# Kernel optimization log

Measured on AMD Instinct MI355X. Metric: run time of the kernel, lower is better.

## Reference

```python
import jax, jax.numpy as jnp
import numpy as np

N_NODES = 50000
N_EDGES = 800000
NUM_FEATURES = 128
HIDDEN = 128


def _gcn_conv(x, src, dst, norm, W, b, num_nodes):
    # x: [N, F_in], W: [F_in, F_out]
    h = x @ W                              # dense transform first (PyG order)
    msg = h[src] * norm[:, None]           # gather + per-edge scale
    out = jax.ops.segment_sum(msg, dst, num_segments=num_nodes)  # scatter-add
    return out + b


def _prep_edges(edge_index, num_nodes):
    # add self loops
    loop = jnp.arange(num_nodes, dtype=edge_index.dtype)
    src = jnp.concatenate([edge_index[0], loop])
    dst = jnp.concatenate([edge_index[1], loop])
    # symmetric normalization deg^{-1/2}[src] * deg^{-1/2}[dst]
    deg = jax.ops.segment_sum(jnp.ones_like(dst, dtype=jnp.float32), dst,
                              num_segments=num_nodes)
    dinv = jnp.where(deg > 0, jax.lax.rsqrt(deg), 0.0)
    norm = dinv[src] * dinv[dst]
    return src, dst, norm


def setup_inputs() -> dict:
    key = jax.random.key(0)
    ks = jax.random.split(key, 5)
    s1 = 1.0 / np.sqrt(NUM_FEATURES)
    s2 = 1.0 / np.sqrt(HIDDEN)
    return {
        "x": jax.random.normal(ks[0], (N_NODES, NUM_FEATURES), jnp.float32),
        "edge_index": jax.random.randint(ks[1], (2, N_EDGES), 0, N_NODES,
                                         dtype=jnp.int64),
        "W1": jax.random.normal(ks[2], (NUM_FEATURES, HIDDEN), jnp.float32) * s1,
        "b1": jnp.zeros((HIDDEN,), jnp.float32),
        "W2": jax.random.normal(ks[3], (HIDDEN, HIDDEN), jnp.float32) * s2,
        "b2": jnp.zeros((HIDDEN,), jnp.float32),
        "Wout": jax.random.normal(ks[4], (HIDDEN, 1), jnp.float32) * s2,
        "bout": jnp.zeros((1,), jnp.float32),
    }


def reference(x, edge_index, W1, b1, W2, b2, Wout, bout):
    num_nodes = x.shape[0]
    src, dst, norm = _prep_edges(edge_index, num_nodes)
    h = _gcn_conv(x, src, dst, norm, W1, b1, num_nodes)
    h = jax.nn.relu(h)
    h = _gcn_conv(h, src, dst, norm, W2, b2, num_nodes)
    h = jax.nn.relu(h)
    return jax.nn.sigmoid(h @ Wout + bout)
```

## Files before the change

### kernel.cpp

```cpp
#include <hip/hip_runtime.h>
#include <math.h>

#define NN 50000
#define NE 800000
#define NBUK 196
#define PBLK 256
#define EPB (NE / PBLK)

typedef __attribute__((ext_vector_type(8))) short bf16x8;
typedef __attribute__((ext_vector_type(4))) float f32x4;

__device__ __forceinline__ unsigned short f2b(float f) {
  union { float f; unsigned u; } v; v.f = f;
  unsigned r = v.u + 0x7FFF + ((v.u >> 16) & 1);
  return (unsigned short)(r >> 16);
}
__device__ __forceinline__ float plo(unsigned v) {
  union { unsigned u; float f; } t; t.u = v << 16; return t.f;
}
__device__ __forceinline__ float phi(unsigned v) {
  union { unsigned u; float f; } t; t.u = v & 0xFFFF0000u; return t.f;
}

__device__ __forceinline__ int edge_val(const void* ei, long long idx, int is64) {
  if (is64) return (int)((const long long*)ei)[idx];
  return ((const int*)ei)[idx];
}

__global__ __launch_bounds__(256) void k_phist(const void* __restrict__ ei,
                                               int* __restrict__ bh) {
  __shared__ int hist[NBUK];
  __shared__ int sflag;
  if (threadIdx.x < 64) {
    unsigned v = ((const unsigned*)ei)[2 * threadIdx.x + 1];
    unsigned long long m = __ballot(v == 0u);
    if (threadIdx.x == 0) sflag = (m == ~0ull) ? 1 : 0;
  }
  if (threadIdx.x < NBUK) hist[threadIdx.x] = 0;
  __syncthreads();
  int is64 = sflag;
  int base = blockIdx.x * EPB;
  for (int e = base + threadIdx.x; e < base + EPB; e += 256) {
    int d = edge_val(ei, (long long)NE + e, is64);
    atomicAdd(&hist[d >> 8], 1);
  }
  __syncthreads();
  if (threadIdx.x < NBUK) bh[threadIdx.x * PBLK + blockIdx.x] = hist[threadIdx.x];
}

__global__ __launch_bounds__(256) void k_pscanA(int* __restrict__ bh,
                                                int* __restrict__ colsum) {
  __shared__ int sh[256];
  int k = blockIdx.x, t = threadIdx.x;
  int v = bh[k * PBLK + t];
  sh[t] = v;
  __syncthreads();
  for (int s = 1; s < 256; s <<= 1) {
    int u = (t >= s) ? sh[t - s] : 0;
    __syncthreads();
    sh[t] += u;
    __syncthreads();
  }
  bh[k * PBLK + t] = sh[t] - v;
  if (t == 255) colsum[k] = sh[255];
}

__global__ __launch_bounds__(256) void k_pscanB(const int* __restrict__ colsum,
                                                int* __restrict__ bstart) {
  __shared__ int sh[256];
  int t = threadIdx.x;
  sh[t] = (t < NBUK) ? colsum[t] : 0;
  __syncthreads();
  for (int s = 1; s < 256; s <<= 1) {
    int u = (t >= s) ? sh[t - s] : 0;
    __syncthreads();
    sh[t] += u;
    __syncthreads();
  }
  if (t <= NBUK) bstart[t] = (t == 0) ? 0 : sh[t - 1];
}

__global__ __launch_bounds__(256) void k_pscat(const void* __restrict__ ei,
                                               const int* __restrict__ bh,
                                               const int* __restrict__ bstart,
                                               unsigned* __restrict__ epk) {
  __shared__ int cur[NBUK];
  __shared__ int sflag;
  if (threadIdx.x < 64) {
    unsigned v = ((const unsigned*)ei)[2 * threadIdx.x + 1];
    unsigned long long m = __ballot(v == 0u);
    if (threadIdx.x == 0) sflag = (m == ~0ull) ? 1 : 0;
  }
  if (threadIdx.x < NBUK)
    cur[threadIdx.x] = bstart[threadIdx.x] + bh[threadIdx.x * PBLK + blockIdx.x];
  __syncthreads();
  int is64 = sflag;
  int base = blockIdx.x * EPB;
  for (int e = base + threadIdx.x; e < base + EPB; e += 256) {
    int d = edge_val(ei, (long long)NE + e, is64);
    int s = edge_val(ei, e, is64);
    int p = atomicAdd(&cur[d >> 8], 1);
    epk[p] = (unsigned)s | ((unsigned)(d & 255) << 16);
  }
}

__global__ __launch_bounds__(256) void k_bofffill(const unsigned* __restrict__ epk,
                                                  const int* __restrict__ bstart,
                                                  int* __restrict__ off,
                                                  float* __restrict__ dinv,
                                                  unsigned short* __restrict__ csr16) {
  __shared__ int hist[256];
  __shared__ int cur[256];
  int k = blockIdx.x, t = threadIdx.x;
  hist[t] = 0;
  __syncthreads();
  int e0 = bstart[k], e1 = bstart[k + 1];
  for (int e = e0 + t; e < e1; e += 256)
    atomicAdd(&hist[(epk[e] >> 16) & 255], 1);
  __syncthreads();
  int myc = hist[t];
  for (int s = 1; s < 256; s <<= 1) {
    int u = (t >= s) ? hist[t - s] : 0;
    __syncthreads();
    hist[t] += u;
    __syncthreads();
  }
  int excl = hist[t] - myc;
  int node = k * 256 + t;
  if (node < NN) {
    off[node] = e0 + excl;
    dinv[node] = rsqrtf((float)(myc + 1));
  }
  cur[t] = e0 + excl;
  __syncthreads();
  for (int e = e0 + t; e < e1; e += 256) {
    unsigned pk = epk[e];
    int p = atomicAdd(&cur[(pk >> 16) & 255], 1);
    csr16[p] = (unsigned short)(pk & 0xFFFFu);
  }
  if (k == 0 && t == 0) off[NN] = NE;
}

__global__ __launch_bounds__(256) void k_wt2(const float* __restrict__ W1,
                                             const float* __restrict__ W2,
                                             unsigned short* __restrict__ Wt1,
                                             unsigned short* __restrict__ Wt2) {
  int i = blockIdx.x * 256 + threadIdx.x;
  int sel = i >> 14;
  int j = i & 16383;
  int k = j >> 7, n = j & 127;
  const float* W = sel ? W2 : W1;
  unsigned short* Wt = sel ? Wt2 : Wt1;
  Wt[n * 128 + k] = f2b(W[j]);
}

template <int A_F32>
__global__ __launch_bounds__(256, 2) void k_mgemm(const void* __restrict__ Ap,
                                                  const unsigned short* __restrict__ Wt,
                                                  const float* __restrict__ dinv,
                                                  unsigned short* __restrict__ Out,
                                                  int M) {
  int wid  = (blockIdx.x * blockDim.x + threadIdx.x) >> 6;
  int lane = threadIdx.x & 63;
  int nw   = (gridDim.x * blockDim.x) >> 6;
  int r  = lane & 15;
  int kg = lane >> 4;
  bf16x8 wf[8][4];
#pragma unroll
  for (int n = 0; n < 8; ++n)
#pragma unroll
    for (int kk = 0; kk < 4; ++kk)
      wf[n][kk] = *(const bf16x8*)&Wt[(n * 16 + r) * 128 + kk * 32 + kg * 8];
  int nstr = M >> 4;
  for (int s = wid; s < nstr; s += nw) {
    int row = s * 16 + r;
    bf16x8 xf[4];
    if (A_F32) {
      const float* Ar = (const float*)Ap + (long long)row * 128 + kg * 8;
#pragma unroll
      for (int kk = 0; kk < 4; ++kk) {
        float4 lo4 = *(const float4*)(Ar + kk * 32);
        float4 hi4 = *(const float4*)(Ar + kk * 32 + 4);
        bf16x8 t;
        t[0] = (short)f2b(lo4.x); t[1] = (short)f2b(lo4.y);
        t[2] = (short)f2b(lo4.z); t[3] = (short)f2b(lo4.w);
        t[4] = (short)f2b(hi4.x); t[5] = (short)f2b(hi4.y);
        t[6] = (short)f2b(hi4.z); t[7] = (short)f2b(hi4.w);
        xf[kk] = t;
      }
    } else {
      const unsigned short* Ar = (const unsigned short*)Ap + (long long)row * 128 + kg * 8;
#pragma unroll
      for (int kk = 0; kk < 4; ++kk)
        xf[kk] = *(const bf16x8*)(Ar + kk * 32);
    }
    f32x4 acc[8];
#pragma unroll
    for (int n = 0; n < 8; ++n) acc[n] = (f32x4){0.f, 0.f, 0.f, 0.f};
#pragma unroll
    for (int kk = 0; kk < 4; ++kk)
#pragma unroll
      for (int n = 0; n < 8; ++n)
        acc[n] = __builtin_amdgcn_mfma_f32_16x16x32_bf16(wf[n][kk], xf[kk], acc[n], 0, 0, 0);
    float dv = dinv[row];
    unsigned short* Or = Out + (long long)row * 128 + kg * 4;
#pragma unroll
    for (int n = 0; n < 8; ++n) {
      uint2 o;
      o.x = (unsigned)f2b(acc[n][0] * dv) | ((unsigned)f2b(acc[n][1] * dv) << 16);
      o.y = (unsigned)f2b(acc[n][2] * dv) | ((unsigned)f2b(acc[n][3] * dv) << 16);
      *(uint2*)(Or + n * 16) = o;
    }
  }
}

template <int FINAL>
__global__ __launch_bounds__(256) void k_agg(const unsigned short* __restrict__ Tb,
                                             const int* __restrict__ off,
                                             const unsigned short* __restrict__ csr16,
                                             const float* __restrict__ dinv,
                                             const float* __restrict__ bias,
                                             const float* __restrict__ wout,
                                             const float* __restrict__ bout,
                                             void* __restrict__ outp) {
  const uint2* Tw2 = (const uint2*)Tb;
  int wid  = (blockIdx.x * blockDim.x + threadIdx.x) >> 6;
  int lane = threadIdx.x & 63;
  int half = lane >> 5;
  int li   = lane & 31;
  int nw   = (gridDim.x * blockDim.x) >> 6;
  float4 b4 = ((const float4*)bias)[li];
  float4 w4 = make_float4(0.f, 0.f, 0.f, 0.f);
  if (FINAL) w4 = ((const float4*)wout)[li];
  for (int d = wid; d < NN; d += nw) {
    int e0 = off[d], e1 = off[d + 1];
    int np  = (e1 - e0) >> 1;
    int rem = (e1 - e0) & 1;
    int s_init = half ? (rem ? (int)csr16[e1 - 1] : -1) : d;
    float a0 = 0.f, a1 = 0.f, a2 = 0.f, a3 = 0.f;
    if (s_init >= 0) {
      uint2 vv = Tw2[s_init * 32 + li];
      a0 = plo(vv.x); a1 = phi(vv.x); a2 = plo(vv.y); a3 = phi(vv.y);
    }
    int st = 0;
    int base = e0 + half;
    for (; st + 4 <= np; st += 4) {
      int s0 = csr16[base + 2 * st];
      int s1 = csr16[base + 2 * st + 2];
      int s2 = csr16[base + 2 * st + 4];
      int s3 = csr16[base + 2 * st + 6];
      uint2 v0 = Tw2[s0 * 32 + li];
      uint2 v1 = Tw2[s1 * 32 + li];
      uint2 v2 = Tw2[s2 * 32 + li];
      uint2 v3 = Tw2[s3 * 32 + li];
      a0 += plo(v0.x); a1 += phi(v0.x); a2 += plo(v0.y); a3 += phi(v0.y);
      a0 += plo(v1.x); a1 += phi(v1.x); a2 += plo(v1.y); a3 += phi(v1.y);
      a0 += plo(v2.x); a1 += phi(v2.x); a2 += plo(v2.y); a3 += phi(v2.y);
      a0 += plo(v3.x); a1 += phi(v3.x); a2 += plo(v3.y); a3 += phi(v3.y);
    }
    for (; st < np; ++st) {
      int s = csr16[base + 2 * st];
      uint2 vv = Tw2[s * 32 + li];
      a0 += plo(vv.x); a1 += phi(vv.x); a2 += plo(vv.y); a3 += phi(vv.y);
    }
    a0 += __shfl_xor(a0, 32, 64);
    a1 += __shfl_xor(a1, 32, 64);
    a2 += __shfl_xor(a2, 32, 64);
    a3 += __shfl_xor(a3, 32, 64);
    float dv = dinv[d];
    a0 = fmaxf(fmaf(a0, dv, b4.x), 0.f);
    a1 = fmaxf(fmaf(a1, dv, b4.y), 0.f);
    a2 = fmaxf(fmaf(a2, dv, b4.z), 0.f);
    a3 = fmaxf(fmaf(a3, dv, b4.w), 0.f);
    if (FINAL) {
      float r = a0 * w4.x + a1 * w4.y + a2 * w4.z + a3 * w4.w;
      r += __shfl_xor(r, 16, 64);
      r += __shfl_xor(r, 8, 64);
      r += __shfl_xor(r, 4, 64);
      r += __shfl_xor(r, 2, 64);
      r += __shfl_xor(r, 1, 64);
      if (lane == 0) ((float*)outp)[d] = 1.f / (1.f + __expf(-(r + bout[0])));
    } else {
      if (half == 0) {
        uint2 o;
        o.x = (unsigned)f2b(a0) | ((unsigned)f2b(a1) << 16);
        o.y = (unsigned)f2b(a2) | ((unsigned)f2b(a3) << 16);
        ((uint2*)outp)[d * 32 + li] = o;
      }
    }
  }
}

extern "C" void kernel_launch(void* const* d_in, const int* in_sizes, int n_in,
                              void* d_out, int out_size, void* d_ws, size_t ws_size,
                              hipStream_t stream) {
  const float* x  = (const float*)d_in[0];
  const void*  ei = d_in[1];
  const float* W1 = (const float*)d_in[2];
  const float* b1 = (const float*)d_in[3];
  const float* W2 = (const float*)d_in[4];
  const float* b2 = (const float*)d_in[5];
  const float* Wo = (const float*)d_in[6];
  const float* bo = (const float*)d_in[7];
  float* out = (float*)d_out;

  char* p = (char*)d_ws;
  auto alloc = [&](size_t bytes) {
    char* r = p;
    p += (bytes + 511) & ~(size_t)511;
    return r;
  };
  int*   bh     = (int*)alloc(sizeof(int) * NBUK * PBLK);
  int*   colsum = (int*)alloc(sizeof(int) * NBUK);
  int*   bstart = (int*)alloc(sizeof(int) * (NBUK + 1));
  int*   off    = (int*)alloc(sizeof(int) * (NN + 1));
  float* dinv   = (float*)alloc(sizeof(float) * NN);
  unsigned short* csr16 = (unsigned short*)alloc(sizeof(short) * NE);
  unsigned short* Wt1 = (unsigned short*)alloc(sizeof(short) * 128 * 128);
  unsigned short* Wt2 = (unsigned short*)alloc(sizeof(short) * 128 * 128);
  unsigned short* T   = (unsigned short*)alloc(sizeof(short) * (size_t)NN * 128);
  unsigned short* H   = (unsigned short*)alloc(sizeof(short) * (size_t)NN * 128);
  unsigned* epk = (unsigned*)T;

  k_phist<<<PBLK, 256, 0, stream>>>(ei, bh);
  k_pscanA<<<NBUK, 256, 0, stream>>>(bh, colsum);
  k_pscanB<<<1, 256, 0, stream>>>(colsum, bstart);
  k_pscat<<<PBLK, 256, 0, stream>>>(ei, bh, bstart, epk);
  k_bofffill<<<NBUK, 256, 0, stream>>>(epk, bstart, off, dinv, csr16);
  k_wt2<<<128, 256, 0, stream>>>(W1, W2, Wt1, Wt2);

  k_mgemm<1><<<512, 256, 0, stream>>>(x, Wt1, dinv, T, NN);
  k_agg<0><<<2048, 256, 0, stream>>>(T, off, csr16, dinv, b1, nullptr, nullptr, H);
  k_mgemm<0><<<512, 256, 0, stream>>>(H, Wt2, dinv, T, NN);
  k_agg<1><<<2048, 256, 0, stream>>>(T, off, csr16, dinv, b2, Wo, bo, out);
}
```

Before: 213.4 us.

## Widen aggregation gathers to 16B per lane and fold weight transpose into histogram

The aggregation kernel now splits each wavefront into four 16-lane groups, each loading a full 256-byte bf16 row with uint4 loads, so four edges are gathered at once instead of two. The partial sums are combined with two shuffle stages. Separately, the weight transpose/convert kernel is folded into the histogram kernel (256 blocks × 128 threads cover both 128x128 matrices), which removes one launch. The wider per-lane loads raise register use and add an extra shuffle stage, and the four groups leave more lanes idle on low-degree nodes.

```diff
diff --git a/kernel.cpp b/kernel.cpp
--- a/kernel.cpp
+++ b/kernel.cpp
@@ -28,7 +28,18 @@
 }
 
 __global__ __launch_bounds__(256) void k_phist(const void* __restrict__ ei,
-                                               int* __restrict__ bh) {
+                                               int* __restrict__ bh,
+                                               const float* __restrict__ W1,
+                                               const float* __restrict__ W2,
+                                               unsigned short* __restrict__ Wt1,
+                                               unsigned short* __restrict__ Wt2) {
+  if (threadIdx.x < 128) {
+    int gi = blockIdx.x * 128 + threadIdx.x;
+    int sel = gi >> 14;
+    int j = gi & 16383;
+    int k = j >> 7, n = j & 127;
+    (sel ? Wt2 : Wt1)[n * 128 + k] = f2b((sel ? W2 : W1)[j]);
+  }
   __shared__ int hist[NBUK];
   __shared__ int sflag;
   if (threadIdx.x < 64) {
@@ -139,19 +150,6 @@
     csr16[p] = (unsigned short)(pk & 0xFFFFu);
   }
   if (k == 0 && t == 0) off[NN] = NE;
-}
-
-__global__ __launch_bounds__(256) void k_wt2(const float* __restrict__ W1,
-                                             const float* __restrict__ W2,
-                                             unsigned short* __restrict__ Wt1,
-                                             unsigned short* __restrict__ Wt2) {
-  int i = blockIdx.x * 256 + threadIdx.x;
-  int sel = i >> 14;
-  int j = i & 16383;
-  int k = j >> 7, n = j & 127;
-  const float* W = sel ? W2 : W1;
-  unsigned short* Wt = sel ? Wt2 : Wt1;
-  Wt[n * 128 + k] = f2b(W[j]);
 }
 
 template <int A_F32>
@@ -223,70 +221,85 @@
                                              const float* __restrict__ wout,
                                              const float* __restrict__ bout,
                                              void* __restrict__ outp) {
-  const uint2* Tw2 = (const uint2*)Tb;
+  const uint4* Tw4 = (const uint4*)Tb;
   int wid  = (blockIdx.x * blockDim.x + threadIdx.x) >> 6;
   int lane = threadIdx.x & 63;
-  int half = lane >> 5;
-  int li   = lane & 31;
+  int grp  = lane >> 4;
+  int li   = lane & 15;
   int nw   = (gridDim.x * blockDim.x) >> 6;
-  float4 b4 = ((const float4*)bias)[li];
-  float4 w4 = make_float4(0.f, 0.f, 0.f, 0.f);
-  if (FINAL) w4 = ((const float4*)wout)[li];
+  float4 bA = ((const float4*)bias)[li * 2];
+  float4 bB = ((const float4*)bias)[li * 2 + 1];
+  float4 wA = make_float4(0.f, 0.f, 0.f, 0.f), wB = wA;
+  if (FINAL) { wA = ((const float4*)wout)[li * 2]; wB = ((const float4*)wout)[li * 2 + 1]; }
   for (int d = wid; d < NN; d += nw) {
     int e0 = off[d], e1 = off[d + 1];
-    int np  = (e1 - e0) >> 1;
-    int rem = (e1 - e0) & 1;
-    int s_init = half ? (rem ? (int)csr16[e1 - 1] : -1) : d;
-    float a0 = 0.f, a1 = 0.f, a2 = 0.f, a3 = 0.f;
+    int ne = e1 - e0;
+    int np = ne >> 2, rem = ne & 3;
+    int s_init = (grp == 0) ? d : ((grp - 1) < rem ? (int)csr16[e1 - 1 - (grp - 1)] : -1);
+    float a0 = 0.f, a1 = 0.f, a2 = 0.f, a3 = 0.f, a4 = 0.f, a5 = 0.f, a6 = 0.f, a7 = 0.f;
     if (s_init >= 0) {
-      uint2 vv = Tw2[s_init * 32 + li];
-      a0 = plo(vv.x); a1 = phi(vv.x); a2 = plo(vv.y); a3 = phi(vv.y);
-    }
+      uint4 v = Tw4[s_init * 16 + li];
+      a0 = plo(v.x); a1 = phi(v.x); a2 = plo(v.y); a3 = phi(v.y);
+      a4 = plo(v.z); a5 = phi(v.z); a6 = plo(v.w); a7 = phi(v.w);
+    }
+    int base = e0 + grp;
     int st = 0;
-    int base = e0 + half;
     for (; st + 4 <= np; st += 4) {
-      int s0 = csr16[base + 2 * st];
-      int s1 = csr16[base + 2 * st + 2];
-      int s2 = csr16[base + 2 * st + 4];
-      int s3 = csr16[base + 2 * st + 6];
-      uint2 v0 = Tw2[s0 * 32 + li];
-      uint2 v1 = Tw2[s1 * 32 + li];
-      uint2 v2 = Tw2[s2 * 32 + li];
-      uint2 v3 = Tw2[s3 * 32 + li];
+      int s0 = csr16[base + 4 * st];
+      int s1 = csr16[base + 4 * st + 4];
+      int s2 = csr16[base + 4 * st + 8];
+      int s3 = csr16[base + 4 * st + 12];
+      uint4 v0 = Tw4[s0 * 16 + li];
+      uint4 v1 = Tw4[s1 * 16 + li];
+      uint4 v2 = Tw4[s2 * 16 + li];
+      uint4 v3 = Tw4[s3 * 16 + li];
       a0 += plo(v0.x); a1 += phi(v0.x); a2 += plo(v0.y); a3 += phi(v0.y);
+      a4 += plo(v0.z); a5 += phi(v0.z); a6 += plo(v0.w); a7 += phi(v0.w);
       a0 += plo(v1.x); a1 += phi(v1.x); a2 += plo(v1.y); a3 += phi(v1.y);
+      a4 += plo(v1.z); a5 += phi(v1.z); a6 += plo(v1.w); a7 += phi(v1.w);
       a0 += plo(v2.x); a1 += phi(v2.x); a2 += plo(v2.y); a3 += phi(v2.y);
+      a4 += plo(v2.z); a5 += phi(v2.z); a6 += plo(v2.w); a7 += phi(v2.w);
       a0 += plo(v3.x); a1 += phi(v3.x); a2 += plo(v3.y); a3 += phi(v3.y);
+      a4 += plo(v3.z); a5 += phi(v3.z); a6 += plo(v3.w); a7 += phi(v3.w);
     }
     for (; st < np; ++st) {
-      int s = csr16[base + 2 * st];
-      uint2 vv = Tw2[s * 32 + li];
-      a0 += plo(vv.x); a1 += phi(vv.x); a2 += plo(vv.y); a3 += phi(vv.y);
-    }
-    a0 += __shfl_xor(a0, 32, 64);
-    a1 += __shfl_xor(a1, 32, 64);
-    a2 += __shfl_xor(a2, 32, 64);
-    a3 += __shfl_xor(a3, 32, 64);
+      int s = csr16[base + 4 * st];
+      uint4 v = Tw4[s * 16 + li];
+      a0 += plo(v.x); a1 += phi(v.x); a2 += plo(v.y); a3 += phi(v.y);
+      a4 += plo(v.z); a5 += phi(v.z); a6 += plo(v.w); a7 += phi(v.w);
+    }
+    a0 += __shfl_xor(a0, 16, 64); a1 += __shfl_xor(a1, 16, 64);
+    a2 += __shfl_xor(a2, 16, 64); a3 += __shfl_xor(a3, 16, 64);
+    a4 += __shfl_xor(a4, 16, 64); a5 += __shfl_xor(a5, 16, 64);
+    a6 += __shfl_xor(a6, 16, 64); a7 += __shfl_xor(a7, 16, 64);
+    a0 += __shfl_xor(a0, 32, 64); a1 += __shfl_xor(a1, 32, 64);
+    a2 += __shfl_xor(a2, 32, 64); a3 += __shfl_xor(a3, 32, 64);
+    a4 += __shfl_xor(a4, 32, 64); a5 += __shfl_xor(a5, 32, 64);
+    a6 += __shfl_xor(a6, 32, 64); a7 += __shfl_xor(a7, 32, 64);
     float dv = dinv[d];
-    a0 = fmaxf(fmaf(a0, dv, b4.x), 0.f);
-    a1 = fmaxf(fmaf(a1, dv, b4.y), 0.f);
-    a2 = fmaxf(fmaf(a2, dv, b4.z), 0.f);
-    a3 = fmaxf(fmaf(a3, dv, b4.w), 0.f);
+    a0 = fmaxf(fmaf(a0, dv, bA.x), 0.f);
+    a1 = fmaxf(fmaf(a1, dv, bA.y), 0.f);
+    a2 = fmaxf(fmaf(a2, dv, bA.z), 0.f);
+    a3 = fmaxf(fmaf(a3, dv, bA.w), 0.f);
+    a4 = fmaxf(fmaf(a4, dv, bB.x), 0.f);
+    a5 = fmaxf(fmaf(a5, dv, bB.y), 0.f);
+    a6 = fmaxf(fmaf(a6, dv, bB.z), 0.f);
+    a7 = fmaxf(fmaf(a7, dv, bB.w), 0.f);
     if (FINAL) {
-      float r = a0 * w4.x + a1 * w4.y + a2 * w4.z + a3 * w4.w;
-      r += __shfl_xor(r, 16, 64);
+      float r = a0 * wA.x + a1 * wA.y + a2 * wA.z + a3 * wA.w
+              + a4 * wB.x + a5 * wB.y + a6 * wB.z + a7 * wB.w;
       r += __shfl_xor(r, 8, 64);
       r += __shfl_xor(r, 4, 64);
       r += __shfl_xor(r, 2, 64);
       r += __shfl_xor(r, 1, 64);
       if (lane == 0) ((float*)outp)[d] = 1.f / (1.f + __expf(-(r + bout[0])));
-    } else {
-      if (half == 0) {
-        uint2 o;
-        o.x = (unsigned)f2b(a0) | ((unsigned)f2b(a1) << 16);
-        o.y = (unsigned)f2b(a2) | ((unsigned)f2b(a3) << 16);
-        ((uint2*)outp)[d * 32 + li] = o;
-      }
+    } else if (grp == 0) {
+      uint4 o;
+      o.x = (unsigned)f2b(a0) | ((unsigned)f2b(a1) << 16);
+      o.y = (unsigned)f2b(a2) | ((unsigned)f2b(a3) << 16);
+      o.z = (unsigned)f2b(a4) | ((unsigned)f2b(a5) << 16);
+      o.w = (unsigned)f2b(a6) | ((unsigned)f2b(a7) << 16);
+      ((uint4*)outp)[d * 16 + li] = o;
     }
   }
 }
@@ -322,12 +335,11 @@
   unsigned short* H   = (unsigned short*)alloc(sizeof(short) * (size_t)NN * 128);
   unsigned* epk = (unsigned*)T;
 
-  k_phist<<<PBLK, 256, 0, stream>>>(ei, bh);
+  k_phist<<<PBLK, 256, 0, stream>>>(ei, bh, W1, W2, Wt1, Wt2);
   k_pscanA<<<NBUK, 256, 0, stream>>>(bh, colsum);
   k_pscanB<<<1, 256, 0, stream>>>(colsum, bstart);
   k_pscat<<<PBLK, 256, 0, stream>>>(ei, bh, bstart, epk);
   k_bofffill<<<NBUK, 256, 0, stream>>>(epk, bstart, off, dinv, csr16);
-  k_wt2<<<128, 256, 0, stream>>>(W1, W2, Wt1, Wt2);
 
   k_mgemm<1><<<512, 256, 0, stream>>>(x, Wt1, dinv, T, NN);
   k_agg<0><<<2048, 256, 0, stream>>>(T, off, csr16, dinv, b1, nullptr, nullptr, H);
```

Result: no change. 216.7 us (+1.5%).
